# Performance work log

Hardware: AMD Instinct MI355X
Metric: run time of the kernel (lower is better)

## Reference

```python
import jax, jax.numpy as jnp
import numpy as np

E = 64          # num experts
IN = 512        # input_size
OUT = 512       # output_size
N = 131072      # total tokens = sum(expert_size)
CAP = 3072      # static per-expert capacity (>= max expert_size)


def _make_expert_sizes():
    # uneven but deterministic sizes summing to N, all <= CAP
    rng = np.random.default_rng(0)
    sizes = np.full(E, N // E, dtype=np.int32)
    d = rng.integers(0, 513, size=E // 2).astype(np.int32)
    sizes[0::2] += d
    sizes[1::2] -= d
    assert sizes.sum() == N and sizes.max() <= CAP and sizes.min() > 0
    return jnp.asarray(sizes, dtype=jnp.int32)


def setup_inputs() -> dict:
    key = jax.random.key(0)
    k1, k2 = jax.random.split(key)
    inputs = jax.random.normal(k1, (N, IN), dtype=jnp.float32)
    # matches nn.init.uniform_(weight, -1/in, 1/in)
    weight = jax.random.uniform(k2, (E, IN, OUT), dtype=jnp.float32,
                                minval=-1.0 / IN, maxval=1.0 / IN)
    expert_size = _make_expert_sizes()
    return {"inputs": inputs, "expert_size": expert_size, "weight": weight}


def reference(inputs, expert_size, weight):
    # Grouped GEMM: tokens are pre-sorted by expert; segment e is
    # inputs[offset[e]:offset[e]+expert_size[e]] @ weight[e].
    cap_ids = jnp.arange(CAP, dtype=jnp.int32)                # [CAP]
    offsets = jnp.cumsum(expert_size) - expert_size           # [E]
    idx = offsets[:, None] + cap_ids[None, :]                 # [E, CAP]
    valid = cap_ids[None, :] < expert_size[:, None]           # [E, CAP]
    idx = jnp.where(valid, idx, N)                            # invalid -> OOB (dropped)
    # gather tokens into padded per-expert blocks; invalid slots -> 0
    x = jnp.take(inputs, idx, axis=0, mode='fill', fill_value=0.0)  # [E, CAP, IN]
    h = jnp.einsum('eci,eio->eco', x, weight)                 # [E, CAP, OUT]
    out = jnp.zeros((N, OUT), dtype=inputs.dtype)
    out = out.at[idx.reshape(-1)].add(h.reshape(-1, OUT), mode='drop')
    return out
```

## Files before the change

kernel.cpp:

```cpp
#include <hip/hip_runtime.h>
#include <hip/hip_bf16.h>

#define E_NUM 64
#define IN_SZ 512
#define OUT_SZ 512
#define N_TOK 131072
#define CAP 3072

#define BM 128
#define BN 256
#define BK 32
#define THREADS 256
#define RT_MAX 24
#define CT_NUM 2

typedef __attribute__((ext_vector_type(8))) short short8;
typedef __attribute__((ext_vector_type(4))) float f32x4;

__device__ inline unsigned short f2bf(float f) {
    unsigned int u = __float_as_uint(f);
    unsigned int r = (u + 0x7FFF + ((u >> 16) & 1)) >> 16;
    return (unsigned short)r;
}

#define GLOAD_LDS16(g, l)                                                     \
    __builtin_amdgcn_global_load_lds(                                         \
        (const __attribute__((address_space(1))) void*)(g),                   \
        (__attribute__((address_space(3))) void*)(l), 16, 0, 0)

__global__ void offsets_kernel(const int* __restrict__ sizes, int* __restrict__ offs) {
    int e = threadIdx.x;
    int s = 0;
    for (int i = 0; i < e; ++i) s += sizes[i];
    offs[e] = s;
}

__global__ __launch_bounds__(256) void prep_wt(const float* __restrict__ W,
                                               unsigned short* __restrict__ WT) {
    __shared__ float t[32][33];
    int k0 = blockIdx.x * 32, n0 = blockIdx.y * 32, e = blockIdx.z;
    const float* We = W + (size_t)e * IN_SZ * OUT_SZ;
    int tid = threadIdx.x;
    int r = tid >> 3, c4 = (tid & 7) * 4;
    float4 v = *(const float4*)(We + (size_t)(k0 + r) * OUT_SZ + n0 + c4);
    t[r][c4 + 0] = v.x; t[r][c4 + 1] = v.y; t[r][c4 + 2] = v.z; t[r][c4 + 3] = v.w;
    __syncthreads();
    ushort4 o;
    o.x = f2bf(t[c4 + 0][r]);
    o.y = f2bf(t[c4 + 1][r]);
    o.z = f2bf(t[c4 + 2][r]);
    o.w = f2bf(t[c4 + 3][r]);
    unsigned short* O = WT + (size_t)e * IN_SZ * OUT_SZ + (size_t)(n0 + r) * IN_SZ + k0 + c4;
    *(ushort4*)O = o;
}

__global__ __launch_bounds__(THREADS, 2) void gemm_moe(
    const float* __restrict__ A, const int* __restrict__ sizes,
    const unsigned short* __restrict__ WT, const int* __restrict__ offs,
    float* __restrict__ out)
{
    int b0 = blockIdx.x;
    int wg = (b0 & 7) * (E_NUM * RT_MAX * CT_NUM / 8) + (b0 >> 3);
    int ct = wg & (CT_NUM - 1);
    int rt = (wg >> 1) % RT_MAX;
    int e  = wg / (RT_MAX * CT_NUM);

    int size_e = sizes[e];
    int rows0 = rt * BM;
    if (rows0 >= size_e) return;
    int off_e = offs[e];
    int rows_rem = size_e - rows0;
    int maxr = (rows_rem < BM ? rows_rem : BM) - 1;

    __shared__ unsigned short lsA[2][BM * BK];
    __shared__ unsigned short lsB[2][BN * BK];

    int tid = threadIdx.x, l = tid & 63, w = tid >> 6;
    const char* WTe = (const char*)(WT + (size_t)e * IN_SZ * OUT_SZ);
    const float* Abase = A + (size_t)(off_e + rows0) * IN_SZ;

    float4 ar[4];

    auto loadA = [&](int kt) {
        #pragma unroll
        for (int i = 0; i < 4; ++i) {
            int idx = tid + THREADS * i;
            int row = idx >> 3, c4 = idx & 7;
            int gr = row <= maxr ? row : maxr;
            ar[i] = *(const float4*)(Abase + (size_t)gr * IN_SZ + kt * BK + c4 * 4);
        }
    };
    auto writeA = [&](int buf) {
        #pragma unroll
        for (int i = 0; i < 4; ++i) {
            int idx = tid + THREADS * i;
            int row = idx >> 3, cb = (idx & 7) * 8;
            int cbs = cb ^ ((((row >> 1) & 3)) << 4);
            ushort4 p;
            p.x = f2bf(ar[i].x); p.y = f2bf(ar[i].y);
            p.z = f2bf(ar[i].z); p.w = f2bf(ar[i].w);
            *(ushort4*)((char*)&lsA[buf][0] + row * 64 + cbs) = p;
        }
    };
    auto stageB = [&](int buf, int kt) {
        #pragma unroll
        for (int i = 0; i < 4; ++i) {
            int j = (w * 4 + i) * 1024 + l * 16;
            int n = j >> 6, c = j & 63;
            int csrc = c ^ ((((n >> 1) & 3)) << 4);
            const char* g = WTe + (size_t)(ct * BN + n) * (IN_SZ * 2) + kt * 64 + csrc;
            GLOAD_LDS16(g, &lsB[buf][(w * 4 + i) * 512]);
        }
    };

    loadA(0);
    stageB(0, 0);
    writeA(0);
    __syncthreads();

    f32x4 acc[4][8] = {};
    int wm = (w >> 1) * 64, wn = (w & 1) * 128;
    int lrow = l & 15;
    int cb = ((l >> 4) * 16) ^ ((((lrow >> 1) & 3)) << 4);

    for (int kt = 0; kt < IN_SZ / BK; ++kt) {
        int cur = kt & 1;
        if (kt < IN_SZ / BK - 1) {
            loadA(kt + 1);
            stageB(cur ^ 1, kt + 1);
        }
        const char* pA = (const char*)&lsA[cur][0];
        const char* pB = (const char*)&lsB[cur][0];
        short8 af[4];
        #pragma unroll
        for (int m = 0; m < 4; ++m)
            af[m] = *(const short8*)(pA + (wm + m * 16 + lrow) * 64 + cb);
        #pragma unroll
        for (int nh = 0; nh < 2; ++nh) {
            short8 bfr[4];
            #pragma unroll
            for (int n2 = 0; n2 < 4; ++n2)
                bfr[n2] = *(const short8*)(pB + (wn + nh * 64 + n2 * 16 + lrow) * 64 + cb);
            #pragma unroll
            for (int m = 0; m < 4; ++m)
                #pragma unroll
                for (int n2 = 0; n2 < 4; ++n2)
                    acc[m][nh * 4 + n2] = __builtin_amdgcn_mfma_f32_16x16x32_bf16(
                        af[m], bfr[n2], acc[m][nh * 4 + n2], 0, 0, 0);
        }
        if (kt < IN_SZ / BK - 1)
            writeA(cur ^ 1);
        __syncthreads();
    }

    float* outb = out + (size_t)(off_e + rows0) * OUT_SZ + ct * BN + wn;
    #pragma unroll
    for (int m = 0; m < 4; ++m) {
        #pragma unroll
        for (int j = 0; j < 4; ++j) {
            int rl = wm + m * 16 + (l >> 4) * 4 + j;
            if (rl < rows_rem) {
                float* po = outb + (size_t)rl * OUT_SZ + (l & 15);
                #pragma unroll
                for (int n = 0; n < 8; ++n)
                    po[n * 16] = acc[m][n][j];
            }
        }
    }
}

extern "C" void kernel_launch(void* const* d_in, const int* in_sizes, int n_in,
                              void* d_out, int out_size, void* d_ws, size_t ws_size,
                              hipStream_t stream) {
    const float* A      = (const float*)d_in[0];
    const int* sizes    = (const int*)d_in[1];
    const float* W      = (const float*)d_in[2];
    float* out          = (float*)d_out;

    unsigned short* WT  = (unsigned short*)d_ws;
    int* offs           = (int*)((char*)d_ws + (size_t)E_NUM * IN_SZ * OUT_SZ * 2);

    offsets_kernel<<<1, E_NUM, 0, stream>>>(sizes, offs);
    prep_wt<<<dim3(IN_SZ / 32, OUT_SZ / 32, E_NUM), 256, 0, stream>>>(W, WT);
    gemm_moe<<<E_NUM * RT_MAX * CT_NUM, THREADS, 0, stream>>>(A, sizes, WT, offs, out);
}
```

Baseline: 197.7 us.

## Load MFMA operands directly from global memory into registers, bypassing LDS

Drops the shared-memory staging for both A and B tiles. Each lane now loads its MFMA fragments straight from global memory into registers, with a fully unrolled register double buffer and no block barriers. The fp32-to-bf16 conversion of A now uses the packed v_cvt_pk_bf16_f32 instruction instead of manual rounding. The cost is lost data sharing inside the block: each wave reloads A and B rows that other waves also need. That raises global and L2 traffic and register pressure, and the per-lane accesses are strided and poorly coalesced.

```diff
diff --git a/kernel.cpp b/kernel.cpp
--- a/kernel.cpp
+++ b/kernel.cpp
@@ -9,13 +9,14 @@
 
 #define BM 128
 #define BN 256
-#define BK 32
 #define THREADS 256
 #define RT_MAX 24
 #define CT_NUM 2
+#define JT 16
 
 typedef __attribute__((ext_vector_type(8))) short short8;
 typedef __attribute__((ext_vector_type(4))) float f32x4;
+typedef __attribute__((ext_vector_type(4))) unsigned int u32x4;
 
 __device__ inline unsigned short f2bf(float f) {
     unsigned int u = __float_as_uint(f);
@@ -23,10 +24,11 @@
     return (unsigned short)r;
 }
 
-#define GLOAD_LDS16(g, l)                                                     \
-    __builtin_amdgcn_global_load_lds(                                         \
-        (const __attribute__((address_space(1))) void*)(g),                   \
-        (__attribute__((address_space(3))) void*)(l), 16, 0, 0)
+__device__ inline unsigned int cvtpk(float a, float b) {
+    unsigned int r;
+    asm("v_cvt_pk_bf16_f32 %0, %1, %2" : "=v"(r) : "v"(a), "v"(b));
+    return r;
+}
 
 __global__ void offsets_kernel(const int* __restrict__ sizes, int* __restrict__ offs) {
     int e = threadIdx.x;
@@ -72,85 +74,63 @@
     int rows_rem = size_e - rows0;
     int maxr = (rows_rem < BM ? rows_rem : BM) - 1;
 
-    __shared__ unsigned short lsA[2][BM * BK];
-    __shared__ unsigned short lsB[2][BN * BK];
+    int tid = threadIdx.x, l = tid & 63, w = tid >> 6;
+    int wm = (w >> 1) * 64, wn = (w & 1) * 128;
+    int lrow = l & 15, kq = l >> 4;
 
-    int tid = threadIdx.x, l = tid & 63, w = tid >> 6;
-    const char* WTe = (const char*)(WT + (size_t)e * IN_SZ * OUT_SZ);
-    const float* Abase = A + (size_t)(off_e + rows0) * IN_SZ;
+    const char* Abase = (const char*)(A + (size_t)(off_e + rows0) * IN_SZ);
+    const char* Bbase = (const char*)WT + (size_t)e * IN_SZ * OUT_SZ * 2
+                      + (size_t)(ct * BN + wn + lrow) * (IN_SZ * 2) + kq * 16;
 
-    float4 ar[4];
+    int aoff[4];
+    #pragma unroll
+    for (int m = 0; m < 4; ++m) {
+        int r = wm + m * 16 + lrow;
+        r = r <= maxr ? r : maxr;
+        aoff[m] = r * (IN_SZ * 4) + kq * 32;
+    }
 
-    auto loadA = [&](int kt) {
-        #pragma unroll
-        for (int i = 0; i < 4; ++i) {
-            int idx = tid + THREADS * i;
-            int row = idx >> 3, c4 = idx & 7;
-            int gr = row <= maxr ? row : maxr;
-            ar[i] = *(const float4*)(Abase + (size_t)gr * IN_SZ + kt * BK + c4 * 4);
+    f32x4 ar[4][2];
+    short8 br[2][8];
+
+    #define LOADA(kt)                                                         \
+        _Pragma("unroll")                                                     \
+        for (int m = 0; m < 4; ++m) {                                         \
+            ar[m][0] = *(const f32x4*)(Abase + aoff[m] + (kt) * 128);         \
+            ar[m][1] = *(const f32x4*)(Abase + aoff[m] + (kt) * 128 + 16);    \
         }
-    };
-    auto writeA = [&](int buf) {
-        #pragma unroll
-        for (int i = 0; i < 4; ++i) {
-            int idx = tid + THREADS * i;
-            int row = idx >> 3, cb = (idx & 7) * 8;
-            int cbs = cb ^ ((((row >> 1) & 3)) << 4);
-            ushort4 p;
-            p.x = f2bf(ar[i].x); p.y = f2bf(ar[i].y);
-            p.z = f2bf(ar[i].z); p.w = f2bf(ar[i].w);
-            *(ushort4*)((char*)&lsA[buf][0] + row * 64 + cbs) = p;
-        }
-    };
-    auto stageB = [&](int buf, int kt) {
-        #pragma unroll
-        for (int i = 0; i < 4; ++i) {
-            int j = (w * 4 + i) * 1024 + l * 16;
-            int n = j >> 6, c = j & 63;
-            int csrc = c ^ ((((n >> 1) & 3)) << 4);
-            const char* g = WTe + (size_t)(ct * BN + n) * (IN_SZ * 2) + kt * 64 + csrc;
-            GLOAD_LDS16(g, &lsB[buf][(w * 4 + i) * 512]);
-        }
-    };
-
-    loadA(0);
-    stageB(0, 0);
-    writeA(0);
-    __syncthreads();
+    #define LOADB(kt, s)                                                      \
+        _Pragma("unroll")                                                     \
+        for (int n = 0; n < 8; ++n)                                           \
+            br[s][n] = *(const short8*)(Bbase + n * (16 * IN_SZ * 2) + (kt) * 64);
 
     f32x4 acc[4][8] = {};
-    int wm = (w >> 1) * 64, wn = (w & 1) * 128;
-    int lrow = l & 15;
-    int cb = ((l >> 4) * 16) ^ ((((lrow >> 1) & 3)) << 4);
 
-    for (int kt = 0; kt < IN_SZ / BK; ++kt) {
-        int cur = kt & 1;
-        if (kt < IN_SZ / BK - 1) {
-            loadA(kt + 1);
-            stageB(cur ^ 1, kt + 1);
+    LOADA(0);
+    LOADB(0, 0);
+
+    #pragma unroll
+    for (int kt = 0; kt < JT; ++kt) {
+        u32x4 au[4];
+        #pragma unroll
+        for (int m = 0; m < 4; ++m) {
+            au[m][0] = cvtpk(ar[m][0][0], ar[m][0][1]);
+            au[m][1] = cvtpk(ar[m][0][2], ar[m][0][3]);
+            au[m][2] = cvtpk(ar[m][1][0], ar[m][1][1]);
+            au[m][3] = cvtpk(ar[m][1][2], ar[m][1][3]);
         }
-        const char* pA = (const char*)&lsA[cur][0];
-        const char* pB = (const char*)&lsB[cur][0];
-        short8 af[4];
+        if (kt + 1 < JT) {
+            LOADA(kt + 1);
+            LOADB(kt + 1, (kt + 1) & 1);
+        }
         #pragma unroll
-        for (int m = 0; m < 4; ++m)
-            af[m] = *(const short8*)(pA + (wm + m * 16 + lrow) * 64 + cb);
-        #pragma unroll
-        for (int nh = 0; nh < 2; ++nh) {
-            short8 bfr[4];
+        for (int m = 0; m < 4; ++m) {
+            short8 af = __builtin_bit_cast(short8, au[m]);
             #pragma unroll
-            for (int n2 = 0; n2 < 4; ++n2)
-                bfr[n2] = *(const short8*)(pB + (wn + nh * 64 + n2 * 16 + lrow) * 64 + cb);
-            #pragma unroll
-            for (int m = 0; m < 4; ++m)
-                #pragma unroll
-                for (int n2 = 0; n2 < 4; ++n2)
-                    acc[m][nh * 4 + n2] = __builtin_amdgcn_mfma_f32_16x16x32_bf16(
-                        af[m], bfr[n2], acc[m][nh * 4 + n2], 0, 0, 0);
+            for (int n = 0; n < 8; ++n)
+                acc[m][n] = __builtin_amdgcn_mfma_f32_16x16x32_bf16(
+                    af, br[kt & 1][n], acc[m][n], 0, 0, 0);
         }
-        if (kt < IN_SZ / BK - 1)
-            writeA(cur ^ 1);
-        __syncthreads();
     }
 
     float* outb = out + (size_t)(off_e + rows0) * OUT_SZ + ct * BN + wn;
@@ -158,9 +138,9 @@
     for (int m = 0; m < 4; ++m) {
         #pragma unroll
         for (int j = 0; j < 4; ++j) {
-            int rl = wm + m * 16 + (l >> 4) * 4 + j;
+            int rl = wm + m * 16 + kq * 4 + j;
             if (rl < rows_rem) {
-                float* po = outb + (size_t)rl * OUT_SZ + (l & 15);
+                float* po = outb + (size_t)rl * OUT_SZ + lrow;
                 #pragma unroll
                 for (int n = 0; n < 8; ++n)
                     po[n * 16] = acc[m][n][j];
```

Measured after the change: 370.4 us. 87.3% more time.
